# Performance work log

Hardware: AMD Instinct MI355X
Metric: run time of the kernel (lower is better)

Reference implementation:

```python
import jax, jax.numpy as jnp
import numpy as np
import math

N = 1024
C = 128
H = 4
HD = C // H  # 32
HID = C // 2  # geom_mlp hidden


def setup_inputs() -> dict:
    key = jax.random.key(0)
    ks = jax.random.split(key, 12)
    s = 0.02
    return {
        "x": jax.random.normal(ks[0], (N, C), jnp.float32),
        "y": jax.random.normal(ks[1], (N, C), jnp.float32),
        "pos": jax.random.normal(ks[2], (N, 3), jnp.float32),
        "Wq": jax.random.normal(ks[3], (C, C), jnp.float32) * s,
        "bq": jnp.zeros((C,), jnp.float32),
        "Wk": jax.random.normal(ks[4], (C, C), jnp.float32) * s,
        "bk": jnp.zeros((C,), jnp.float32),
        "Wv": jax.random.normal(ks[5], (C, C), jnp.float32) * s,
        "bv": jnp.zeros((C,), jnp.float32),
        "W1": jax.random.normal(ks[6], (3, HID), jnp.float32) * s,
        "b1": jnp.zeros((HID,), jnp.float32),
        "W2": jax.random.normal(ks[7], (HID, C), jnp.float32) * s,
        "b2": jnp.zeros((C,), jnp.float32),
    }


def _safe_norm(sq):
    # sqrt with zero (sub)gradient at 0, matching torch.norm behavior
    pos_mask = sq > 0
    return jnp.where(pos_mask, jnp.sqrt(jnp.where(pos_mask, sq, 1.0)), 0.0)


def reference(x, y, pos, Wq, bq, Wk, bk, Wv, bv, W1, b1, W2, b2):
    # pairwise geometry
    pos_diff = pos[:, None, :] - pos[None, :, :]          # [N, N, 3]
    dist = _safe_norm(jnp.sum(pos_diff * pos_diff, -1))   # [N, N]
    geom = jax.nn.relu(pos_diff @ W1 + b1) @ W2 + b2      # [N, N, C]
    geom = geom.reshape(N, N, H, HD)                      # per-head split

    q = (x @ Wq + bq).reshape(N, H, HD)
    k = (y @ Wk + bk).reshape(N, H, HD)
    v = (y @ Wv + bv).reshape(N, H, HD)

    attn = jnp.einsum("ihd,jhd->hij", q, k) / math.sqrt(HD)  # [H, N, N]
    geom_attn = jnp.einsum("ihd,ijhd->hij", q, geom)         # [H, N, N]
    scores = attn + geom_attn - dist[None, :, :]
    p = jax.nn.softmax(scores, axis=-1)
    out = jnp.einsum("hij,jhd->ihd", p, v).reshape(N, C)     # [N, C]
    return out
```

## Files before the change

### kernel.cpp

```cpp
#include <hip/hip_runtime.h>
#include <math.h>


typedef float v2f __attribute__((ext_vector_type(2)));
typedef float v4f __attribute__((ext_vector_type(4)));

#define L2E 1.4426950408889634f
#define RSL (0.17677669529663687f * L2E)

static __device__ __forceinline__ float dot4(float4 a, float4 b) {
  return a.x*b.x + a.y*b.y + a.z*b.z + a.w*b.w;
}
static __device__ __forceinline__ v2f fma2(v2f a, v2f b, v2f c) {
  return __builtin_elementwise_fma(a, b, c);
}
static __device__ __forceinline__ v4f fma4s(float s, v4f b, v4f c) {
  v4f sv = {s, s, s, s};
  return __builtin_elementwise_fma(sv, b, c);
}

__global__ __launch_bounds__(384) void k_pre(
    const float* __restrict__ x, const float* __restrict__ y, const float* __restrict__ pos,
    const float* __restrict__ Wq, const float* __restrict__ bq,
    const float* __restrict__ Wk, const float* __restrict__ bk,
    const float* __restrict__ Wv, const float* __restrict__ bv,
    const float* __restrict__ W1, const float* __restrict__ b1,
    const float* __restrict__ W2, const float* __restrict__ b2,
    float* __restrict__ q, float* __restrict__ v,
    float* __restrict__ kT4f, float* __restrict__ uT4f,
    float* __restrict__ sA, float* __restrict__ pos4w)
{
  __shared__ float xs[256], ys[256], qs[256];
  __shared__ __align__(16) float4 W2S[64*33];

  const int t  = threadIdx.x;
  const int n0 = blockIdx.x * 2;

  if (t < 256) { xs[t] = x[n0*128 + t]; ys[t] = y[n0*128 + t]; }
  {
    const float4* w2g = (const float4*)W2;
    #pragma unroll
    for (int r = 0; r < 6; ++r) {
      const int e = t + 384*r;
      if (e < 2048) W2S[(e>>5)*33 + (e&31)] = w2g[e];
    }
  }
  __syncthreads();

  {
    const int c   = t & 127;
    const int mat = t >> 7;
    const float* W    = (mat == 0) ? Wq : (mat == 1 ? Wk : Wv);
    const float* S    = (mat == 0) ? xs : ys;
    const float* bias = (mat == 0) ? bq : (mat == 1 ? bk : bv);
    float a0 = 0.f, a1 = 0.f;
    #pragma unroll 8
    for (int d = 0; d < 128; ++d) {
      const float w_ = W[d*128 + c];
      a0 = fmaf(S[d],       w_, a0);
      a1 = fmaf(S[128 + d], w_, a1);
    }
    const float bb = bias[c];
    a0 += bb; a1 += bb;
    if (mat == 0) {
      q[n0*128 + c] = a0 * RSL; q[(n0+1)*128 + c] = a1 * RSL;
      qs[c] = a0; qs[128 + c] = a1;
    } else if (mat == 2) {
      v[n0*128 + c] = a0; v[(n0+1)*128 + c] = a1;
    } else {
      kT4f[((c>>2)*1024 + n0  )*4 + (c&3)] = a0;
      kT4f[((c>>2)*1024 + n0+1)*4 + (c&3)] = a1;
    }
  }
  __syncthreads();

  if (t < 256) {
    const int m = t & 63, h = t >> 6;
    const float4* qs4 = (const float4*)qs;
    #pragma unroll
    for (int ii = 0; ii < 2; ++ii) {
      float acc = 0.f;
      #pragma unroll
      for (int ch = 0; ch < 8; ++ch)
        acc += dot4(qs4[ii*32 + h*8 + ch], W2S[m*33 + h*8 + ch]);
      sA[(n0+ii)*328 + 8 + (m>>2)*20 + h*4 + (m&3)] = acc * L2E;
    }
    if (t < 8) {
      const int ii = t >> 2, h2 = t & 3;
      float ca = 0.f;
      #pragma unroll
      for (int d = 0; d < 32; ++d) ca = fmaf(qs[ii*128 + h2*32 + d], b2[h2*32 + d], ca);
      sA[(n0+ii)*328 + h2] = ca * L2E;
    } else if (t < 16) {
      const int tt = t-8, ii = tt>>2, cc = tt&3;
      sA[(n0+ii)*328 + 4 + cc] = (cc < 3) ? pos[(n0+ii)*3 + cc] * L2E : 0.f;
    } else if (t < 24) {
      const int tt = t-16, ii = tt>>2, cc = tt&3;
      pos4w[(n0+ii)*4 + cc] = (cc < 3) ? pos[(n0+ii)*3 + cc] * L2E : 0.f;
    }
  } else {
    const int tt = t - 256, ii = tt >> 6, m = tt & 63;
    float ua = 0.f;
    #pragma unroll
    for (int cc = 0; cc < 3; ++cc) ua = fmaf(pos[(n0+ii)*3 + cc], W1[cc*64 + m], ua);
    uT4f[((m>>2)*1024 + (n0+ii))*4 + (m&3)] = ua;
    sA[(n0+ii)*328 + 8 + (m>>2)*20 + 16 + (m&3)] = ua + b1[m];
  }
}

__global__ __launch_bounds__(512, 4) void k_attn(
    const float* __restrict__ q, const float* __restrict__ v,
    const v4f* __restrict__ kT4, const v4f* __restrict__ uT4,
    const float* __restrict__ sA, const v4f* __restrict__ pos4,
    float* __restrict__ out)
{
  __shared__ __align__(16) float eL[8*544];
  __shared__ __align__(16) float rnum[4096];
  __shared__ float rden[64];

  const int t    = threadIdx.x;
  const int i0   = blockIdx.x * 2;
  const int w    = t >> 6;
  const int lane = t & 63;
  const int c4   = lane & 31;
  const int rep  = lane >> 5;
  const int hh   = c4 >> 3;

  const float* sA0 = sA + i0*328;
  const float* sA1 = sA0 + 328;
  const float* q0  = q + i0*128;
  const float* q1  = q0 + 128;

  const float c00 = sA0[0], c01 = sA0[1], c02 = sA0[2], c03 = sA0[3];
  const float c10 = sA1[0], c11 = sA1[1], c12 = sA1[2], c13 = sA1[3];
  const float p0x = sA0[4], p0y = sA0[5], p0z = sA0[6];
  const float p1x = sA1[4], p1y = sA1[5], p1z = sA1[6];

  v4f acc0 = {0.f,0.f,0.f,0.f};
  v4f acc1 = {0.f,0.f,0.f,0.f};
  float lsum[8] = {0.f,0.f,0.f,0.f,0.f,0.f,0.f,0.f};

  float* eW = &eL[w*544];
  const v4f* er0 = (const v4f*)&eL[w*544 +  hh     *68 + rep*32];
  const v4f* er1 = (const v4f*)&eL[w*544 + (4+hh)  *68 + rep*32];

  #pragma unroll
  for (int tt2 = 0; tt2 < 2; ++tt2) {
    const int jb = (w*2 + tt2) * 64;
    const int j  = jb + lane;

    const v4f pj = pos4[j];
    const float d0x = p0x-pj.x, d0y = p0y-pj.y, d0z = p0z-pj.z;
    const float d1x = p1x-pj.x, d1y = p1y-pj.y, d1z = p1z-pj.z;
    const float dist0 = sqrtf(d0x*d0x + d0y*d0y + d0z*d0z);
    const float dist1 = sqrtf(d1x*d1x + d1y*d1y + d1z*d1z);

    v2f g0a={0.f,0.f}, g0b={0.f,0.f}, g0c={0.f,0.f}, g0d={0.f,0.f};
    v2f g1a={0.f,0.f}, g1b={0.f,0.f}, g1c={0.f,0.f}, g1d={0.f,0.f};
    #pragma unroll 4
    for (int mb = 0; mb < 16; ++mb) {
      const v4f uj = uT4[mb*1024 + j];
      const v2f uj01 = uj.xy, uj23 = uj.zw;
      {
        const float* ab = sA0 + 8 + mb*20;
        const v2f z = {0.f, 0.f};
        const v2f h01 = __builtin_elementwise_max(*(const v2f*)(ab+16) - uj01, z);
        const v2f h23 = __builtin_elementwise_max(*(const v2f*)(ab+18) - uj23, z);
        g0a = fma2(h01, *(const v2f*)(ab+ 0), g0a); g0a = fma2(h23, *(const v2f*)(ab+ 2), g0a);
        g0b = fma2(h01, *(const v2f*)(ab+ 4), g0b); g0b = fma2(h23, *(const v2f*)(ab+ 6), g0b);
        g0c = fma2(h01, *(const v2f*)(ab+ 8), g0c); g0c = fma2(h23, *(const v2f*)(ab+10), g0c);
        g0d = fma2(h01, *(const v2f*)(ab+12), g0d); g0d = fma2(h23, *(const v2f*)(ab+14), g0d);
      }
      {
        const float* ab = sA1 + 8 + mb*20;
        const v2f z = {0.f, 0.f};
        const v2f h01 = __builtin_elementwise_max(*(const v2f*)(ab+16) - uj01, z);
        const v2f h23 = __builtin_elementwise_max(*(const v2f*)(ab+18) - uj23, z);
        g1a = fma2(h01, *(const v2f*)(ab+ 0), g1a); g1a = fma2(h23, *(const v2f*)(ab+ 2), g1a);
        g1b = fma2(h01, *(const v2f*)(ab+ 4), g1b); g1b = fma2(h23, *(const v2f*)(ab+ 6), g1b);
        g1c = fma2(h01, *(const v2f*)(ab+ 8), g1c); g1c = fma2(h23, *(const v2f*)(ab+10), g1c);
        g1d = fma2(h01, *(const v2f*)(ab+12), g1d); g1d = fma2(h23, *(const v2f*)(ab+14), g1d);
      }
    }

    v2f s0a={0.f,0.f}, s0b={0.f,0.f}, s0c={0.f,0.f}, s0d={0.f,0.f};
    v2f s1a={0.f,0.f}, s1b={0.f,0.f}, s1c={0.f,0.f}, s1d={0.f,0.f};
    #pragma unroll 8
    for (int cb = 0; cb < 8; ++cb) {
      const v4f k0 = kT4[(cb     )*1024 + j];
      const v4f k1 = kT4[(cb +  8)*1024 + j];
      const v4f k2 = kT4[(cb + 16)*1024 + j];
      const v4f k3 = kT4[(cb + 24)*1024 + j];
      s0a = fma2(k0.xy, *(const v2f*)(q0 + cb*4      ), s0a); s0a = fma2(k0.zw, *(const v2f*)(q0 + cb*4 +  2), s0a);
      s0b = fma2(k1.xy, *(const v2f*)(q0 + cb*4 + 32 ), s0b); s0b = fma2(k1.zw, *(const v2f*)(q0 + cb*4 + 34), s0b);
      s0c = fma2(k2.xy, *(const v2f*)(q0 + cb*4 + 64 ), s0c); s0c = fma2(k2.zw, *(const v2f*)(q0 + cb*4 + 66), s0c);
      s0d = fma2(k3.xy, *(const v2f*)(q0 + cb*4 + 96 ), s0d); s0d = fma2(k3.zw, *(const v2f*)(q0 + cb*4 + 98), s0d);
      s1a = fma2(k0.xy, *(const v2f*)(q1 + cb*4      ), s1a); s1a = fma2(k0.zw, *(const v2f*)(q1 + cb*4 +  2), s1a);
      s1b = fma2(k1.xy, *(const v2f*)(q1 + cb*4 + 32 ), s1b); s1b = fma2(k1.zw, *(const v2f*)(q1 + cb*4 + 34), s1b);
      s1c = fma2(k2.xy, *(const v2f*)(q1 + cb*4 + 64 ), s1c); s1c = fma2(k2.zw, *(const v2f*)(q1 + cb*4 + 66), s1c);
      s1d = fma2(k3.xy, *(const v2f*)(q1 + cb*4 + 96 ), s1d); s1d = fma2(k3.zw, *(const v2f*)(q1 + cb*4 + 98), s1d);
    }

    {
      const v2f t0a = s0a + g0a, t0b = s0b + g0b, t0c = s0c + g0c, t0d = s0d + g0d;
      const float p0 = exp2f(t0a.x + t0a.y + (c00 - dist0));
      const float p1 = exp2f(t0b.x + t0b.y + (c01 - dist0));
      const float p2 = exp2f(t0c.x + t0c.y + (c02 - dist0));
      const float p3 = exp2f(t0d.x + t0d.y + (c03 - dist0));
      lsum[0] += p0; lsum[1] += p1; lsum[2] += p2; lsum[3] += p3;
      eW[      lane] = p0; eW[ 68 + lane] = p1; eW[136 + lane] = p2; eW[204 + lane] = p3;
      const v2f t1a = s1a + g1a, t1b = s1b + g1b, t1c = s1c + g1c, t1d = s1d + g1d;
      const float r0 = exp2f(t1a.x + t1a.y + (c10 - dist1));
      const float r1 = exp2f(t1b.x + t1b.y + (c11 - dist1));
      const float r2 = exp2f(t1c.x + t1c.y + (c12 - dist1));
      const float r3 = exp2f(t1d.x + t1d.y + (c13 - dist1));
      lsum[4] += r0; lsum[5] += r1; lsum[6] += r2; lsum[7] += r3;
      eW[272 + lane] = r0; eW[340 + lane] = r1; eW[408 + lane] = r2; eW[476 + lane] = r3;
    }
    __builtin_amdgcn_wave_barrier();

    const v4f* vg = (const v4f*)(v + jb*128);
    const int vbase = rep*32*32 + c4;
    #pragma unroll 4
    for (int jj4 = 0; jj4 < 8; ++jj4) {
      const v4f e0 = er0[jj4];
      const v4f e1 = er1[jj4];
      const v4f va = vg[vbase + (jj4*4+0)*32];
      const v4f vb = vg[vbase + (jj4*4+1)*32];
      const v4f vc = vg[vbase + (jj4*4+2)*32];
      const v4f vd = vg[vbase + (jj4*4+3)*32];
      acc0 = fma4s(e0.x, va, acc0); acc1 = fma4s(e1.x, va, acc1);
      acc0 = fma4s(e0.y, vb, acc0); acc1 = fma4s(e1.y, vb, acc1);
      acc0 = fma4s(e0.z, vc, acc0); acc1 = fma4s(e1.z, vc, acc1);
      acc0 = fma4s(e0.w, vd, acc0); acc1 = fma4s(e1.w, vd, acc1);
    }
    __builtin_amdgcn_wave_barrier();
  }

  #pragma unroll
  for (int mm = 1; mm < 64; mm <<= 1) {
    #pragma unroll
    for (int r8 = 0; r8 < 8; ++r8) lsum[r8] += __shfl_xor(lsum[r8], mm);
  }
  ((v4f*)rnum)[((w*2+0)*2 + rep)*32 + c4] = acc0;
  ((v4f*)rnum)[((w*2+1)*2 + rep)*32 + c4] = acc1;
  if (lane == 0) {
    #pragma unroll
    for (int r8 = 0; r8 < 8; ++r8) rden[w*8 + r8] = lsum[r8];
  }
  __syncthreads();

  if (t < 256) {
    const int ii = t >> 7, c = t & 127;
    float num = 0.f, den = 0.f;
    #pragma unroll
    for (int ww = 0; ww < 8; ++ww) {
      num += rnum[((ww*2+ii)*2+0)*128 + c] + rnum[((ww*2+ii)*2+1)*128 + c];
      den += rden[ww*8 + ii*4 + (c>>5)];
    }
    out[(i0+ii)*128 + c] = num / den;
  }
}

extern "C" void kernel_launch(void* const* d_in, const int* in_sizes, int n_in,
                              void* d_out, int out_size, void* d_ws, size_t ws_size,
                              hipStream_t stream) {
  const float* x   = (const float*)d_in[0];
  const float* y   = (const float*)d_in[1];
  const float* pos = (const float*)d_in[2];
  const float* Wq  = (const float*)d_in[3];
  const float* bq  = (const float*)d_in[4];
  const float* Wk  = (const float*)d_in[5];
  const float* bk  = (const float*)d_in[6];
  const float* Wv  = (const float*)d_in[7];
  const float* bv  = (const float*)d_in[8];
  const float* W1  = (const float*)d_in[9];
  const float* b1  = (const float*)d_in[10];
  const float* W2  = (const float*)d_in[11];
  const float* b2  = (const float*)d_in[12];

  float* ws = (float*)d_ws;
  float* q    = ws;
  float* v    = ws + 131072;
  float* kT4f = ws + 262144;
  float* uT4f = ws + 393216;
  float* sA   = ws + 458752;
  float* pos4 = ws + 794624;
  float* out  = (float*)d_out;

  k_pre<<<dim3(512), dim3(384), 0, stream>>>(x, y, pos, Wq, bq, Wk, bk, Wv, bv,
                                             W1, b1, W2, b2,
                                             q, v, kT4f, uT4f, sA, pos4);
  k_attn<<<dim3(512), dim3(512), 0, stream>>>(q, v, (const v4f*)kT4f,
                                              (const v4f*)uT4f, sA,
                                              (const v4f*)pos4, out);
}
```

Before: 117.1 us.

## Process four query rows per block and split keys across two blocks

The attention kernel now handles four query rows per block, so each key, u and v load is reused across four rows instead of two. The key range is split between two blocks with one 64-key tile per wave. Partial numerators and denominators go to a workspace, and a new finalize kernel combines them. The precompute kernel is also changed to four rows per block. This roughly doubles per-thread accumulator registers, which risks lower occupancy or spills, and it adds a kernel launch plus a workspace round trip.

```diff
diff --git a/kernel.cpp b/kernel.cpp
--- a/kernel.cpp
+++ b/kernel.cpp
@@ -30,13 +30,13 @@
     float* __restrict__ kT4f, float* __restrict__ uT4f,
     float* __restrict__ sA, float* __restrict__ pos4w)
 {
-  __shared__ float xs[256], ys[256], qs[256];
+  __shared__ float xs[512], ys[512], qs[512];
   __shared__ __align__(16) float4 W2S[64*33];
 
   const int t  = threadIdx.x;
-  const int n0 = blockIdx.x * 2;
-
-  if (t < 256) { xs[t] = x[n0*128 + t]; ys[t] = y[n0*128 + t]; }
+  const int n0 = blockIdx.x * 4;
+
+  for (int idx = t; idx < 512; idx += 384) { xs[idx] = x[n0*128 + idx]; ys[idx] = y[n0*128 + idx]; }
   {
     const float4* w2g = (const float4*)W2;
     #pragma unroll
@@ -53,23 +53,29 @@
     const float* W    = (mat == 0) ? Wq : (mat == 1 ? Wk : Wv);
     const float* S    = (mat == 0) ? xs : ys;
     const float* bias = (mat == 0) ? bq : (mat == 1 ? bk : bv);
-    float a0 = 0.f, a1 = 0.f;
-    #pragma unroll 8
+    float a0=0.f, a1=0.f, a2=0.f, a3=0.f;
+    #pragma unroll 4
     for (int d = 0; d < 128; ++d) {
       const float w_ = W[d*128 + c];
-      a0 = fmaf(S[d],       w_, a0);
-      a1 = fmaf(S[128 + d], w_, a1);
+      a0 = fmaf(S[d],     w_, a0);
+      a1 = fmaf(S[128+d], w_, a1);
+      a2 = fmaf(S[256+d], w_, a2);
+      a3 = fmaf(S[384+d], w_, a3);
     }
     const float bb = bias[c];
-    a0 += bb; a1 += bb;
+    a0 += bb; a1 += bb; a2 += bb; a3 += bb;
     if (mat == 0) {
-      q[n0*128 + c] = a0 * RSL; q[(n0+1)*128 + c] = a1 * RSL;
-      qs[c] = a0; qs[128 + c] = a1;
+      q[(n0+0)*128+c] = a0*RSL; q[(n0+1)*128+c] = a1*RSL;
+      q[(n0+2)*128+c] = a2*RSL; q[(n0+3)*128+c] = a3*RSL;
+      qs[c] = a0; qs[128+c] = a1; qs[256+c] = a2; qs[384+c] = a3;
     } else if (mat == 2) {
-      v[n0*128 + c] = a0; v[(n0+1)*128 + c] = a1;
+      v[(n0+0)*128+c] = a0; v[(n0+1)*128+c] = a1;
+      v[(n0+2)*128+c] = a2; v[(n0+3)*128+c] = a3;
     } else {
-      kT4f[((c>>2)*1024 + n0  )*4 + (c&3)] = a0;
+      kT4f[((c>>2)*1024 + n0+0)*4 + (c&3)] = a0;
       kT4f[((c>>2)*1024 + n0+1)*4 + (c&3)] = a1;
+      kT4f[((c>>2)*1024 + n0+2)*4 + (c&3)] = a2;
+      kT4f[((c>>2)*1024 + n0+3)*4 + (c&3)] = a3;
     }
   }
   __syncthreads();
@@ -78,33 +84,38 @@
     const int m = t & 63, h = t >> 6;
     const float4* qs4 = (const float4*)qs;
     #pragma unroll
-    for (int ii = 0; ii < 2; ++ii) {
+    for (int ii = 0; ii < 4; ++ii) {
       float acc = 0.f;
       #pragma unroll
       for (int ch = 0; ch < 8; ++ch)
         acc += dot4(qs4[ii*32 + h*8 + ch], W2S[m*33 + h*8 + ch]);
       sA[(n0+ii)*328 + 8 + (m>>2)*20 + h*4 + (m&3)] = acc * L2E;
     }
-    if (t < 8) {
+    if (t < 16) {
       const int ii = t >> 2, h2 = t & 3;
       float ca = 0.f;
       #pragma unroll
       for (int d = 0; d < 32; ++d) ca = fmaf(qs[ii*128 + h2*32 + d], b2[h2*32 + d], ca);
       sA[(n0+ii)*328 + h2] = ca * L2E;
-    } else if (t < 16) {
-      const int tt = t-8, ii = tt>>2, cc = tt&3;
+    } else if (t < 32) {
+      const int tt = t-16, ii = tt>>2, cc = tt&3;
       sA[(n0+ii)*328 + 4 + cc] = (cc < 3) ? pos[(n0+ii)*3 + cc] * L2E : 0.f;
-    } else if (t < 24) {
-      const int tt = t-16, ii = tt>>2, cc = tt&3;
+    } else if (t < 48) {
+      const int tt = t-32, ii = tt>>2, cc = tt&3;
       pos4w[(n0+ii)*4 + cc] = (cc < 3) ? pos[(n0+ii)*3 + cc] * L2E : 0.f;
     }
   } else {
-    const int tt = t - 256, ii = tt >> 6, m = tt & 63;
-    float ua = 0.f;
-    #pragma unroll
-    for (int cc = 0; cc < 3; ++cc) ua = fmaf(pos[(n0+ii)*3 + cc], W1[cc*64 + m], ua);
-    uT4f[((m>>2)*1024 + (n0+ii))*4 + (m&3)] = ua;
-    sA[(n0+ii)*328 + 8 + (m>>2)*20 + 16 + (m&3)] = ua + b1[m];
+    const int tt = t - 256;
+    #pragma unroll
+    for (int rep = 0; rep < 2; ++rep) {
+      const int e = tt + 128*rep;
+      const int ii = e >> 6, m = e & 63;
+      float ua = 0.f;
+      #pragma unroll
+      for (int cc = 0; cc < 3; ++cc) ua = fmaf(pos[(n0+ii)*3 + cc], W1[cc*64 + m], ua);
+      uT4f[((m>>2)*1024 + (n0+ii))*4 + (m&3)] = ua;
+      sA[(n0+ii)*328 + 8 + (m>>2)*20 + 16 + (m&3)] = ua + b1[m];
+    }
   }
 }
 
@@ -112,154 +123,167 @@
     const float* __restrict__ q, const float* __restrict__ v,
     const v4f* __restrict__ kT4, const v4f* __restrict__ uT4,
     const float* __restrict__ sA, const v4f* __restrict__ pos4,
-    float* __restrict__ out)
+    float* __restrict__ wsP)
 {
-  __shared__ __align__(16) float eL[8*544];
-  __shared__ __align__(16) float rnum[4096];
-  __shared__ float rden[64];
-
-  const int t    = threadIdx.x;
-  const int i0   = blockIdx.x * 2;
-  const int w    = t >> 6;
-  const int lane = t & 63;
-  const int c4   = lane & 31;
-  const int rep  = lane >> 5;
-  const int hh   = c4 >> 3;
-
-  const float* sA0 = sA + i0*328;
-  const float* sA1 = sA0 + 328;
-  const float* q0  = q + i0*128;
-  const float* q1  = q0 + 128;
-
-  const float c00 = sA0[0], c01 = sA0[1], c02 = sA0[2], c03 = sA0[3];
-  const float c10 = sA1[0], c11 = sA1[1], c12 = sA1[2], c13 = sA1[3];
-  const float p0x = sA0[4], p0y = sA0[5], p0z = sA0[6];
-  const float p1x = sA1[4], p1y = sA1[5], p1z = sA1[6];
-
-  v4f acc0 = {0.f,0.f,0.f,0.f};
-  v4f acc1 = {0.f,0.f,0.f,0.f};
-  float lsum[8] = {0.f,0.f,0.f,0.f,0.f,0.f,0.f,0.f};
-
-  float* eW = &eL[w*544];
-  const v4f* er0 = (const v4f*)&eL[w*544 +  hh     *68 + rep*32];
-  const v4f* er1 = (const v4f*)&eL[w*544 + (4+hh)  *68 + rep*32];
-
-  #pragma unroll
-  for (int tt2 = 0; tt2 < 2; ++tt2) {
-    const int jb = (w*2 + tt2) * 64;
-    const int j  = jb + lane;
-
-    const v4f pj = pos4[j];
-    const float d0x = p0x-pj.x, d0y = p0y-pj.y, d0z = p0z-pj.z;
-    const float d1x = p1x-pj.x, d1y = p1y-pj.y, d1z = p1z-pj.z;
-    const float dist0 = sqrtf(d0x*d0x + d0y*d0y + d0z*d0z);
-    const float dist1 = sqrtf(d1x*d1x + d1y*d1y + d1z*d1z);
-
-    v2f g0a={0.f,0.f}, g0b={0.f,0.f}, g0c={0.f,0.f}, g0d={0.f,0.f};
-    v2f g1a={0.f,0.f}, g1b={0.f,0.f}, g1c={0.f,0.f}, g1d={0.f,0.f};
-    #pragma unroll 4
-    for (int mb = 0; mb < 16; ++mb) {
-      const v4f uj = uT4[mb*1024 + j];
-      const v2f uj01 = uj.xy, uj23 = uj.zw;
-      {
-        const float* ab = sA0 + 8 + mb*20;
-        const v2f z = {0.f, 0.f};
-        const v2f h01 = __builtin_elementwise_max(*(const v2f*)(ab+16) - uj01, z);
-        const v2f h23 = __builtin_elementwise_max(*(const v2f*)(ab+18) - uj23, z);
-        g0a = fma2(h01, *(const v2f*)(ab+ 0), g0a); g0a = fma2(h23, *(const v2f*)(ab+ 2), g0a);
-        g0b = fma2(h01, *(const v2f*)(ab+ 4), g0b); g0b = fma2(h23, *(const v2f*)(ab+ 6), g0b);
-        g0c = fma2(h01, *(const v2f*)(ab+ 8), g0c); g0c = fma2(h23, *(const v2f*)(ab+10), g0c);
-        g0d = fma2(h01, *(const v2f*)(ab+12), g0d); g0d = fma2(h23, *(const v2f*)(ab+14), g0d);
-      }
-      {
-        const float* ab = sA1 + 8 + mb*20;
-        const v2f z = {0.f, 0.f};
-        const v2f h01 = __builtin_elementwise_max(*(const v2f*)(ab+16) - uj01, z);
-        const v2f h23 = __builtin_elementwise_max(*(const v2f*)(ab+18) - uj23, z);
-        g1a = fma2(h01, *(const v2f*)(ab+ 0), g1a); g1a = fma2(h23, *(const v2f*)(ab+ 2), g1a);
-        g1b = fma2(h01, *(const v2f*)(ab+ 4), g1b); g1b = fma2(h23, *(const v2f*)(ab+ 6), g1b);
-        g1c = fma2(h01, *(const v2f*)(ab+ 8), g1c); g1c = fma2(h23, *(const v2f*)(ab+10), g1c);
-        g1d = fma2(h01, *(const v2f*)(ab+12), g1d); g1d = fma2(h23, *(const v2f*)(ab+14), g1d);
-      }
-    }
-
-    v2f s0a={0.f,0.f}, s0b={0.f,0.f}, s0c={0.f,0.f}, s0d={0.f,0.f};
-    v2f s1a={0.f,0.f}, s1b={0.f,0.f}, s1c={0.f,0.f}, s1d={0.f,0.f};
-    #pragma unroll 8
-    for (int cb = 0; cb < 8; ++cb) {
-      const v4f k0 = kT4[(cb     )*1024 + j];
-      const v4f k1 = kT4[(cb +  8)*1024 + j];
-      const v4f k2 = kT4[(cb + 16)*1024 + j];
-      const v4f k3 = kT4[(cb + 24)*1024 + j];
-      s0a = fma2(k0.xy, *(const v2f*)(q0 + cb*4      ), s0a); s0a = fma2(k0.zw, *(const v2f*)(q0 + cb*4 +  2), s0a);
-      s0b = fma2(k1.xy, *(const v2f*)(q0 + cb*4 + 32 ), s0b); s0b = fma2(k1.zw, *(const v2f*)(q0 + cb*4 + 34), s0b);
-      s0c = fma2(k2.xy, *(const v2f*)(q0 + cb*4 + 64 ), s0c); s0c = fma2(k2.zw, *(const v2f*)(q0 + cb*4 + 66), s0c);
-      s0d = fma2(k3.xy, *(const v2f*)(q0 + cb*4 + 96 ), s0d); s0d = fma2(k3.zw, *(const v2f*)(q0 + cb*4 + 98), s0d);
-      s1a = fma2(k0.xy, *(const v2f*)(q1 + cb*4      ), s1a); s1a = fma2(k0.zw, *(const v2f*)(q1 + cb*4 +  2), s1a);
-      s1b = fma2(k1.xy, *(const v2f*)(q1 + cb*4 + 32 ), s1b); s1b = fma2(k1.zw, *(const v2f*)(q1 + cb*4 + 34), s1b);
-      s1c = fma2(k2.xy, *(const v2f*)(q1 + cb*4 + 64 ), s1c); s1c = fma2(k2.zw, *(const v2f*)(q1 + cb*4 + 66), s1c);
-      s1d = fma2(k3.xy, *(const v2f*)(q1 + cb*4 + 96 ), s1d); s1d = fma2(k3.zw, *(const v2f*)(q1 + cb*4 + 98), s1d);
-    }
-
-    {
-      const v2f t0a = s0a + g0a, t0b = s0b + g0b, t0c = s0c + g0c, t0d = s0d + g0d;
-      const float p0 = exp2f(t0a.x + t0a.y + (c00 - dist0));
-      const float p1 = exp2f(t0b.x + t0b.y + (c01 - dist0));
-      const float p2 = exp2f(t0c.x + t0c.y + (c02 - dist0));
-      const float p3 = exp2f(t0d.x + t0d.y + (c03 - dist0));
-      lsum[0] += p0; lsum[1] += p1; lsum[2] += p2; lsum[3] += p3;
-      eW[      lane] = p0; eW[ 68 + lane] = p1; eW[136 + lane] = p2; eW[204 + lane] = p3;
-      const v2f t1a = s1a + g1a, t1b = s1b + g1b, t1c = s1c + g1c, t1d = s1d + g1d;
-      const float r0 = exp2f(t1a.x + t1a.y + (c10 - dist1));
-      const float r1 = exp2f(t1b.x + t1b.y + (c11 - dist1));
-      const float r2 = exp2f(t1c.x + t1c.y + (c12 - dist1));
-      const float r3 = exp2f(t1d.x + t1d.y + (c13 - dist1));
-      lsum[4] += r0; lsum[5] += r1; lsum[6] += r2; lsum[7] += r3;
-      eW[272 + lane] = r0; eW[340 + lane] = r1; eW[408 + lane] = r2; eW[476 + lane] = r3;
-    }
-    __builtin_amdgcn_wave_barrier();
-
+  __shared__ __align__(16) float eL[8*1088];
+  __shared__ __align__(16) float rnum[8192];
+  __shared__ float rden[128];
+
+  const int t     = threadIdx.x;
+  const int i0    = (blockIdx.x >> 1) * 4;
+  const int jhalf = blockIdx.x & 1;
+  const int w     = t >> 6;
+  const int lane  = t & 63;
+  const int c4    = lane & 31;
+  const int rep   = lane >> 5;
+  const int hh    = c4 >> 3;
+
+  const int jt = jhalf*8 + w;
+  const int jb = jt*64;
+  const int j  = jb + lane;
+
+  const float* sAi[4];
+  const float* qi[4];
+  #pragma unroll
+  for (int ii = 0; ii < 4; ++ii) { sAi[ii] = sA + (i0+ii)*328; qi[ii] = q + (i0+ii)*128; }
+
+  const v4f pj = pos4[j];
+  float dist[4];
+  #pragma unroll
+  for (int ii = 0; ii < 4; ++ii) {
+    const float dx = sAi[ii][4]-pj.x, dy = sAi[ii][5]-pj.y, dz = sAi[ii][6]-pj.z;
+    dist[ii] = sqrtf(dx*dx + dy*dy + dz*dz);
+  }
+
+  v2f g[4][4];
+  #pragma unroll
+  for (int ii = 0; ii < 4; ++ii)
+    #pragma unroll
+    for (int h = 0; h < 4; ++h) g[ii][h] = (v2f){0.f, 0.f};
+
+  #pragma unroll 4
+  for (int mb = 0; mb < 16; ++mb) {
+    const v4f uj = uT4[mb*1024 + j];
+    const v2f uj01 = uj.xy, uj23 = uj.zw;
+    const v2f z = {0.f, 0.f};
+    #pragma unroll
+    for (int ii = 0; ii < 4; ++ii) {
+      const float* ab = sAi[ii] + 8 + mb*20;
+      const v2f h01 = __builtin_elementwise_max(*(const v2f*)(ab+16) - uj01, z);
+      const v2f h23 = __builtin_elementwise_max(*(const v2f*)(ab+18) - uj23, z);
+      g[ii][0] = fma2(h01, *(const v2f*)(ab+ 0), g[ii][0]); g[ii][0] = fma2(h23, *(const v2f*)(ab+ 2), g[ii][0]);
+      g[ii][1] = fma2(h01, *(const v2f*)(ab+ 4), g[ii][1]); g[ii][1] = fma2(h23, *(const v2f*)(ab+ 6), g[ii][1]);
+      g[ii][2] = fma2(h01, *(const v2f*)(ab+ 8), g[ii][2]); g[ii][2] = fma2(h23, *(const v2f*)(ab+10), g[ii][2]);
+      g[ii][3] = fma2(h01, *(const v2f*)(ab+12), g[ii][3]); g[ii][3] = fma2(h23, *(const v2f*)(ab+14), g[ii][3]);
+    }
+  }
+
+  v2f s[4][4];
+  #pragma unroll
+  for (int ii = 0; ii < 4; ++ii)
+    #pragma unroll
+    for (int h = 0; h < 4; ++h) s[ii][h] = (v2f){0.f, 0.f};
+
+  #pragma unroll 4
+  for (int cb = 0; cb < 8; ++cb) {
+    const v4f k0 = kT4[(cb     )*1024 + j];
+    const v4f k1 = kT4[(cb +  8)*1024 + j];
+    const v4f k2 = kT4[(cb + 16)*1024 + j];
+    const v4f k3 = kT4[(cb + 24)*1024 + j];
+    #pragma unroll
+    for (int ii = 0; ii < 4; ++ii) {
+      const float* qq = qi[ii] + cb*4;
+      s[ii][0] = fma2(k0.xy, *(const v2f*)(qq     ), s[ii][0]); s[ii][0] = fma2(k0.zw, *(const v2f*)(qq +  2), s[ii][0]);
+      s[ii][1] = fma2(k1.xy, *(const v2f*)(qq + 32), s[ii][1]); s[ii][1] = fma2(k1.zw, *(const v2f*)(qq + 34), s[ii][1]);
+      s[ii][2] = fma2(k2.xy, *(const v2f*)(qq + 64), s[ii][2]); s[ii][2] = fma2(k2.zw, *(const v2f*)(qq + 66), s[ii][2]);
+      s[ii][3] = fma2(k3.xy, *(const v2f*)(qq + 96), s[ii][3]); s[ii][3] = fma2(k3.zw, *(const v2f*)(qq + 98), s[ii][3]);
+    }
+  }
+
+  float lsum[16];
+  float* eW = &eL[w*1088];
+  #pragma unroll
+  for (int ii = 0; ii < 4; ++ii) {
+    #pragma unroll
+    for (int h = 0; h < 4; ++h) {
+      const v2f tt = s[ii][h] + g[ii][h];
+      const float p = exp2f(tt.x + tt.y + (sAi[ii][h] - dist[ii]));
+      lsum[ii*4+h] = p;
+      eW[(ii*4+h)*68 + lane] = p;
+    }
+  }
+  __builtin_amdgcn_wave_barrier();
+
+  v4f acc[4] = {{0.f,0.f,0.f,0.f},{0.f,0.f,0.f,0.f},{0.f,0.f,0.f,0.f},{0.f,0.f,0.f,0.f}};
+  {
     const v4f* vg = (const v4f*)(v + jb*128);
     const int vbase = rep*32*32 + c4;
+    const v4f* er[4];
+    #pragma unroll
+    for (int ii = 0; ii < 4; ++ii)
+      er[ii] = (const v4f*)&eL[w*1088 + (ii*4+hh)*68 + rep*32];
     #pragma unroll 4
     for (int jj4 = 0; jj4 < 8; ++jj4) {
-      const v4f e0 = er0[jj4];
-      const v4f e1 = er1[jj4];
       const v4f va = vg[vbase + (jj4*4+0)*32];
       const v4f vb = vg[vbase + (jj4*4+1)*32];
       const v4f vc = vg[vbase + (jj4*4+2)*32];
       const v4f vd = vg[vbase + (jj4*4+3)*32];
-      acc0 = fma4s(e0.x, va, acc0); acc1 = fma4s(e1.x, va, acc1);
-      acc0 = fma4s(e0.y, vb, acc0); acc1 = fma4s(e1.y, vb, acc1);
-      acc0 = fma4s(e0.z, vc, acc0); acc1 = fma4s(e1.z, vc, acc1);
-      acc0 = fma4s(e0.w, vd, acc0); acc1 = fma4s(e1.w, vd, acc1);
-    }
-    __builtin_amdgcn_wave_barrier();
-  }
-
-  #pragma unroll
-  for (int mm = 1; mm < 64; mm <<= 1) {
-    #pragma unroll
-    for (int r8 = 0; r8 < 8; ++r8) lsum[r8] += __shfl_xor(lsum[r8], mm);
-  }
-  ((v4f*)rnum)[((w*2+0)*2 + rep)*32 + c4] = acc0;
-  ((v4f*)rnum)[((w*2+1)*2 + rep)*32 + c4] = acc1;
+      #pragma unroll
+      for (int ii = 0; ii < 4; ++ii) {
+        const v4f e4 = er[ii][jj4];
+        acc[ii] = fma4s(e4.x, va, acc[ii]);
+        acc[ii] = fma4s(e4.y, vb, acc[ii]);
+        acc[ii] = fma4s(e4.z, vc, acc[ii]);
+        acc[ii] = fma4s(e4.w, vd, acc[ii]);
+      }
+    }
+  }
+  __builtin_amdgcn_wave_barrier();
+
+  #pragma unroll
+  for (int mm = 1; mm < 64; mm <<= 1)
+    #pragma unroll
+    for (int r16 = 0; r16 < 16; ++r16) lsum[r16] += __shfl_xor(lsum[r16], mm);
+
+  #pragma unroll
+  for (int ii = 0; ii < 4; ++ii)
+    ((v4f*)rnum)[((w*4 + ii)*2 + rep)*32 + c4] = acc[ii];
   if (lane == 0) {
     #pragma unroll
-    for (int r8 = 0; r8 < 8; ++r8) rden[w*8 + r8] = lsum[r8];
+    for (int r16 = 0; r16 < 16; ++r16) rden[w*16 + r16] = lsum[r16];
   }
   __syncthreads();
 
-  if (t < 256) {
+  float* P = wsP + (size_t)blockIdx.x * 528;
+  {
     const int ii = t >> 7, c = t & 127;
-    float num = 0.f, den = 0.f;
+    float num = 0.f;
     #pragma unroll
     for (int ww = 0; ww < 8; ++ww) {
-      num += rnum[((ww*2+ii)*2+0)*128 + c] + rnum[((ww*2+ii)*2+1)*128 + c];
-      den += rden[ww*8 + ii*4 + (c>>5)];
-    }
-    out[(i0+ii)*128 + c] = num / den;
-  }
+      num += rnum[((ww*4+ii)*2+0)*128 + c];
+      num += rnum[((ww*4+ii)*2+1)*128 + c];
+    }
+    P[ii*128 + c] = num;
+  }
+  if (t < 16) {
+    float den = 0.f;
+    #pragma unroll
+    for (int ww = 0; ww < 8; ++ww) den += rden[ww*16 + t];
+    P[512 + t] = den;
+  }
+}
+
+__global__ __launch_bounds__(512) void k_fin(const float* __restrict__ wsP,
+                                             float* __restrict__ out)
+{
+  const int gid = blockIdx.x * 512 + threadIdx.x;
+  const int i = gid >> 7, c = gid & 127;
+  const int gq = i >> 2, ii = i & 3;
+  const float* P0 = wsP + (size_t)(gq*2+0) * 528;
+  const float* P1 = wsP + (size_t)(gq*2+1) * 528;
+  const float num = P0[ii*128 + c] + P1[ii*128 + c];
+  const float den = P0[512 + ii*4 + (c>>5)] + P1[512 + ii*4 + (c>>5)];
+  out[gid] = num / den;
 }
 
 extern "C" void kernel_launch(void* const* d_in, const int* in_sizes, int n_in,
@@ -286,12 +310,14 @@
   float* uT4f = ws + 393216;
   float* sA   = ws + 458752;
   float* pos4 = ws + 794624;
+  float* wsP  = ws + 798720;
   float* out  = (float*)d_out;
 
-  k_pre<<<dim3(512), dim3(384), 0, stream>>>(x, y, pos, Wq, bq, Wk, bk, Wv, bv,
+  k_pre<<<dim3(256), dim3(384), 0, stream>>>(x, y, pos, Wq, bq, Wk, bk, Wv, bv,
                                              W1, b1, W2, b2,
                                              q, v, kT4f, uT4f, sA, pos4);
   k_attn<<<dim3(512), dim3(512), 0, stream>>>(q, v, (const v4f*)kT4f,
                                               (const v4f*)uT4f, sA,
-                                              (const v4f*)pos4, out);
-}
+                                              (const v4f*)pos4, wsP);
+  k_fin<<<dim3(256), dim3(512), 0, stream>>>(wsP, out);
+}
```

Measured after the change: 141.8 us. +21.0%, slower.

## Split attention key range across two blocks and combine partials in finalize kernel

Applied to the files above, without the earlier changes.

Each query pair is now handled by two blocks, each covering half of the 1024 keys, so every wave processes one 64-key tile instead of looping over two. Partial numerators and denominators go to workspace, and a new finalize kernel sums them and divides. This doubles the grid to 1024 blocks and raises the launch-bounds occupancy hint to improve latency hiding. The cost is an extra kernel launch and a round trip of partial results through global memory.

```diff
diff --git a/kernel.cpp b/kernel.cpp
--- a/kernel.cpp
+++ b/kernel.cpp
@@ -108,23 +108,28 @@
   }
 }
 
-__global__ __launch_bounds__(512, 4) void k_attn(
+__global__ __launch_bounds__(512, 8) void k_attn(
     const float* __restrict__ q, const float* __restrict__ v,
     const v4f* __restrict__ kT4, const v4f* __restrict__ uT4,
     const float* __restrict__ sA, const v4f* __restrict__ pos4,
-    float* __restrict__ out)
+    float* __restrict__ wsP)
 {
   __shared__ __align__(16) float eL[8*544];
   __shared__ __align__(16) float rnum[4096];
   __shared__ float rden[64];
 
-  const int t    = threadIdx.x;
-  const int i0   = blockIdx.x * 2;
-  const int w    = t >> 6;
-  const int lane = t & 63;
-  const int c4   = lane & 31;
-  const int rep  = lane >> 5;
-  const int hh   = c4 >> 3;
+  const int t     = threadIdx.x;
+  const int i0    = (blockIdx.x >> 1) * 2;
+  const int jhalf = blockIdx.x & 1;
+  const int w     = t >> 6;
+  const int lane  = t & 63;
+  const int c4    = lane & 31;
+  const int rep   = lane >> 5;
+  const int hh    = c4 >> 3;
+
+  const int jt = jhalf*8 + w;
+  const int jb = jt*64;
+  const int j  = jb + lane;
 
   const float* sA0 = sA + i0*328;
   const float* sA1 = sA0 + 328;
@@ -136,89 +141,82 @@
   const float p0x = sA0[4], p0y = sA0[5], p0z = sA0[6];
   const float p1x = sA1[4], p1y = sA1[5], p1z = sA1[6];
 
+  const v4f pj = pos4[j];
+  const float d0x = p0x-pj.x, d0y = p0y-pj.y, d0z = p0z-pj.z;
+  const float d1x = p1x-pj.x, d1y = p1y-pj.y, d1z = p1z-pj.z;
+  const float dist0 = sqrtf(d0x*d0x + d0y*d0y + d0z*d0z);
+  const float dist1 = sqrtf(d1x*d1x + d1y*d1y + d1z*d1z);
+
+  v2f g0a={0.f,0.f}, g0b={0.f,0.f}, g0c={0.f,0.f}, g0d={0.f,0.f};
+  v2f g1a={0.f,0.f}, g1b={0.f,0.f}, g1c={0.f,0.f}, g1d={0.f,0.f};
+  #pragma unroll 4
+  for (int mb = 0; mb < 16; ++mb) {
+    const v4f uj = uT4[mb*1024 + j];
+    const v2f uj01 = uj.xy, uj23 = uj.zw;
+    const v2f z = {0.f, 0.f};
+    {
+      const float* ab = sA0 + 8 + mb*20;
+      const v2f h01 = __builtin_elementwise_max(*(const v2f*)(ab+16) - uj01, z);
+      const v2f h23 = __builtin_elementwise_max(*(const v2f*)(ab+18) - uj23, z);
+      g0a = fma2(h01, *(const v2f*)(ab+ 0), g0a); g0a = fma2(h23, *(const v2f*)(ab+ 2), g0a);
+      g0b = fma2(h01, *(const v2f*)(ab+ 4), g0b); g0b = fma2(h23, *(const v2f*)(ab+ 6), g0b);
+      g0c = fma2(h01, *(const v2f*)(ab+ 8), g0c); g0c = fma2(h23, *(const v2f*)(ab+10), g0c);
+      g0d = fma2(h01, *(const v2f*)(ab+12), g0d); g0d = fma2(h23, *(const v2f*)(ab+14), g0d);
+    }
+    {
+      const float* ab = sA1 + 8 + mb*20;
+      const v2f h01 = __builtin_elementwise_max(*(const v2f*)(ab+16) - uj01, z);
+      const v2f h23 = __builtin_elementwise_max(*(const v2f*)(ab+18) - uj23, z);
+      g1a = fma2(h01, *(const v2f*)(ab+ 0), g1a); g1a = fma2(h23, *(const v2f*)(ab+ 2), g1a);
+      g1b = fma2(h01, *(const v2f*)(ab+ 4), g1b); g1b = fma2(h23, *(const v2f*)(ab+ 6), g1b);
+      g1c = fma2(h01, *(const v2f*)(ab+ 8), g1c); g1c = fma2(h23, *(const v2f*)(ab+10), g1c);
+      g1d = fma2(h01, *(const v2f*)(ab+12), g1d); g1d = fma2(h23, *(const v2f*)(ab+14), g1d);
+    }
+  }
+
+  v2f s0a={0.f,0.f}, s0b={0.f,0.f}, s0c={0.f,0.f}, s0d={0.f,0.f};
+  v2f s1a={0.f,0.f}, s1b={0.f,0.f}, s1c={0.f,0.f}, s1d={0.f,0.f};
+  #pragma unroll 8
+  for (int cb = 0; cb < 8; ++cb) {
+    const v4f k0 = kT4[(cb     )*1024 + j];
+    const v4f k1 = kT4[(cb +  8)*1024 + j];
+    const v4f k2 = kT4[(cb + 16)*1024 + j];
+    const v4f k3 = kT4[(cb + 24)*1024 + j];
+    s0a = fma2(k0.xy, *(const v2f*)(q0 + cb*4      ), s0a); s0a = fma2(k0.zw, *(const v2f*)(q0 + cb*4 +  2), s0a);
+    s0b = fma2(k1.xy, *(const v2f*)(q0 + cb*4 + 32 ), s0b); s0b = fma2(k1.zw, *(const v2f*)(q0 + cb*4 + 34), s0b);
+    s0c = fma2(k2.xy, *(const v2f*)(q0 + cb*4 + 64 ), s0c); s0c = fma2(k2.zw, *(const v2f*)(q0 + cb*4 + 66), s0c);
+    s0d = fma2(k3.xy, *(const v2f*)(q0 + cb*4 + 96 ), s0d); s0d = fma2(k3.zw, *(const v2f*)(q0 + cb*4 + 98), s0d);
+    s1a = fma2(k0.xy, *(const v2f*)(q1 + cb*4      ), s1a); s1a = fma2(k0.zw, *(const v2f*)(q1 + cb*4 +  2), s1a);
+    s1b = fma2(k1.xy, *(const v2f*)(q1 + cb*4 + 32 ), s1b); s1b = fma2(k1.zw, *(const v2f*)(q1 + cb*4 + 34), s1b);
+    s1c = fma2(k2.xy, *(const v2f*)(q1 + cb*4 + 64 ), s1c); s1c = fma2(k2.zw, *(const v2f*)(q1 + cb*4 + 66), s1c);
+    s1d = fma2(k3.xy, *(const v2f*)(q1 + cb*4 + 96 ), s1d); s1d = fma2(k3.zw, *(const v2f*)(q1 + cb*4 + 98), s1d);
+  }
+
+  float lsum[8];
+  float* eW = &eL[w*544];
+  {
+    const v2f t0a = s0a + g0a, t0b = s0b + g0b, t0c = s0c + g0c, t0d = s0d + g0d;
+    const float p0 = exp2f(t0a.x + t0a.y + (c00 - dist0));
+    const float p1 = exp2f(t0b.x + t0b.y + (c01 - dist0));
+    const float p2 = exp2f(t0c.x + t0c.y + (c02 - dist0));
+    const float p3 = exp2f(t0d.x + t0d.y + (c03 - dist0));
+    lsum[0] = p0; lsum[1] = p1; lsum[2] = p2; lsum[3] = p3;
+    eW[      lane] = p0; eW[ 68 + lane] = p1; eW[136 + lane] = p2; eW[204 + lane] = p3;
+    const v2f t1a = s1a + g1a, t1b = s1b + g1b, t1c = s1c + g1c, t1d = s1d + g1d;
+    const float r0 = exp2f(t1a.x + t1a.y + (c10 - dist1));
+    const float r1 = exp2f(t1b.x + t1b.y + (c11 - dist1));
+    const float r2 = exp2f(t1c.x + t1c.y + (c12 - dist1));
+    const float r3 = exp2f(t1d.x + t1d.y + (c13 - dist1));
+    lsum[4] = r0; lsum[5] = r1; lsum[6] = r2; lsum[7] = r3;
+    eW[272 + lane] = r0; eW[340 + lane] = r1; eW[408 + lane] = r2; eW[476 + lane] = r3;
+  }
+  __builtin_amdgcn_wave_barrier();
+
   v4f acc0 = {0.f,0.f,0.f,0.f};
   v4f acc1 = {0.f,0.f,0.f,0.f};
-  float lsum[8] = {0.f,0.f,0.f,0.f,0.f,0.f,0.f,0.f};
-
-  float* eW = &eL[w*544];
-  const v4f* er0 = (const v4f*)&eL[w*544 +  hh     *68 + rep*32];
-  const v4f* er1 = (const v4f*)&eL[w*544 + (4+hh)  *68 + rep*32];
-
-  #pragma unroll
-  for (int tt2 = 0; tt2 < 2; ++tt2) {
-    const int jb = (w*2 + tt2) * 64;
-    const int j  = jb + lane;
-
-    const v4f pj = pos4[j];
-    const float d0x = p0x-pj.x, d0y = p0y-pj.y, d0z = p0z-pj.z;
-    const float d1x = p1x-pj.x, d1y = p1y-pj.y, d1z = p1z-pj.z;
-    const float dist0 = sqrtf(d0x*d0x + d0y*d0y + d0z*d0z);
-    const float dist1 = sqrtf(d1x*d1x + d1y*d1y + d1z*d1z);
-
-    v2f g0a={0.f,0.f}, g0b={0.f,0.f}, g0c={0.f,0.f}, g0d={0.f,0.f};
-    v2f g1a={0.f,0.f}, g1b={0.f,0.f}, g1c={0.f,0.f}, g1d={0.f,0.f};
-    #pragma unroll 4
-    for (int mb = 0; mb < 16; ++mb) {
-      const v4f uj = uT4[mb*1024 + j];
-      const v2f uj01 = uj.xy, uj23 = uj.zw;
-      {
-        const float* ab = sA0 + 8 + mb*20;
-        const v2f z = {0.f, 0.f};
-        const v2f h01 = __builtin_elementwise_max(*(const v2f*)(ab+16) - uj01, z);
-        const v2f h23 = __builtin_elementwise_max(*(const v2f*)(ab+18) - uj23, z);
-        g0a = fma2(h01, *(const v2f*)(ab+ 0), g0a); g0a = fma2(h23, *(const v2f*)(ab+ 2), g0a);
-        g0b = fma2(h01, *(const v2f*)(ab+ 4), g0b); g0b = fma2(h23, *(const v2f*)(ab+ 6), g0b);
-        g0c = fma2(h01, *(const v2f*)(ab+ 8), g0c); g0c = fma2(h23, *(const v2f*)(ab+10), g0c);
-        g0d = fma2(h01, *(const v2f*)(ab+12), g0d); g0d = fma2(h23, *(const v2f*)(ab+14), g0d);
-      }
-      {
-        const float* ab = sA1 + 8 + mb*20;
-        const v2f z = {0.f, 0.f};
-        const v2f h01 = __builtin_elementwise_max(*(const v2f*)(ab+16) - uj01, z);
-        const v2f h23 = __builtin_elementwise_max(*(const v2f*)(ab+18) - uj23, z);
-        g1a = fma2(h01, *(const v2f*)(ab+ 0), g1a); g1a = fma2(h23, *(const v2f*)(ab+ 2), g1a);
-        g1b = fma2(h01, *(const v2f*)(ab+ 4), g1b); g1b = fma2(h23, *(const v2f*)(ab+ 6), g1b);
-        g1c = fma2(h01, *(const v2f*)(ab+ 8), g1c); g1c = fma2(h23, *(const v2f*)(ab+10), g1c);
-        g1d = fma2(h01, *(const v2f*)(ab+12), g1d); g1d = fma2(h23, *(const v2f*)(ab+14), g1d);
-      }
-    }
-
-    v2f s0a={0.f,0.f}, s0b={0.f,0.f}, s0c={0.f,0.f}, s0d={0.f,0.f};
-    v2f s1a={0.f,0.f}, s1b={0.f,0.f}, s1c={0.f,0.f}, s1d={0.f,0.f};
-    #pragma unroll 8
-    for (int cb = 0; cb < 8; ++cb) {
-      const v4f k0 = kT4[(cb     )*1024 + j];
-      const v4f k1 = kT4[(cb +  8)*1024 + j];
-      const v4f k2 = kT4[(cb + 16)*1024 + j];
-      const v4f k3 = kT4[(cb + 24)*1024 + j];
-      s0a = fma2(k0.xy, *(const v2f*)(q0 + cb*4      ), s0a); s0a = fma2(k0.zw, *(const v2f*)(q0 + cb*4 +  2), s0a);
-      s0b = fma2(k1.xy, *(const v2f*)(q0 + cb*4 + 32 ), s0b); s0b = fma2(k1.zw, *(const v2f*)(q0 + cb*4 + 34), s0b);
-      s0c = fma2(k2.xy, *(const v2f*)(q0 + cb*4 + 64 ), s0c); s0c = fma2(k2.zw, *(const v2f*)(q0 + cb*4 + 66), s0c);
-      s0d = fma2(k3.xy, *(const v2f*)(q0 + cb*4 + 96 ), s0d); s0d = fma2(k3.zw, *(const v2f*)(q0 + cb*4 + 98), s0d);
-      s1a = fma2(k0.xy, *(const v2f*)(q1 + cb*4      ), s1a); s1a = fma2(k0.zw, *(const v2f*)(q1 + cb*4 +  2), s1a);
-      s1b = fma2(k1.xy, *(const v2f*)(q1 + cb*4 + 32 ), s1b); s1b = fma2(k1.zw, *(const v2f*)(q1 + cb*4 + 34), s1b);
-      s1c = fma2(k2.xy, *(const v2f*)(q1 + cb*4 + 64 ), s1c); s1c = fma2(k2.zw, *(const v2f*)(q1 + cb*4 + 66), s1c);
-      s1d = fma2(k3.xy, *(const v2f*)(q1 + cb*4 + 96 ), s1d); s1d = fma2(k3.zw, *(const v2f*)(q1 + cb*4 + 98), s1d);
-    }
-
-    {
-      const v2f t0a = s0a + g0a, t0b = s0b + g0b, t0c = s0c + g0c, t0d = s0d + g0d;
-      const float p0 = exp2f(t0a.x + t0a.y + (c00 - dist0));
-      const float p1 = exp2f(t0b.x + t0b.y + (c01 - dist0));
-      const float p2 = exp2f(t0c.x + t0c.y + (c02 - dist0));
-      const float p3 = exp2f(t0d.x + t0d.y + (c03 - dist0));
-      lsum[0] += p0; lsum[1] += p1; lsum[2] += p2; lsum[3] += p3;
-      eW[      lane] = p0; eW[ 68 + lane] = p1; eW[136 + lane] = p2; eW[204 + lane] = p3;
-      const v2f t1a = s1a + g1a, t1b = s1b + g1b, t1c = s1c + g1c, t1d = s1d + g1d;
-      const float r0 = exp2f(t1a.x + t1a.y + (c10 - dist1));
-      const float r1 = exp2f(t1b.x + t1b.y + (c11 - dist1));
-      const float r2 = exp2f(t1c.x + t1c.y + (c12 - dist1));
-      const float r3 = exp2f(t1d.x + t1d.y + (c13 - dist1));
-      lsum[4] += r0; lsum[5] += r1; lsum[6] += r2; lsum[7] += r3;
-      eW[272 + lane] = r0; eW[340 + lane] = r1; eW[408 + lane] = r2; eW[476 + lane] = r3;
-    }
-    __builtin_amdgcn_wave_barrier();
-
+  {
+    const v4f* er0 = (const v4f*)&eL[w*544 +  hh    *68 + rep*32];
+    const v4f* er1 = (const v4f*)&eL[w*544 + (4+hh) *68 + rep*32];
     const v4f* vg = (const v4f*)(v + jb*128);
     const int vbase = rep*32*32 + c4;
     #pragma unroll 4
@@ -234,8 +232,8 @@
       acc0 = fma4s(e0.z, vc, acc0); acc1 = fma4s(e1.z, vc, acc1);
       acc0 = fma4s(e0.w, vd, acc0); acc1 = fma4s(e1.w, vd, acc1);
     }
-    __builtin_amdgcn_wave_barrier();
-  }
+  }
+  __builtin_amdgcn_wave_barrier();
 
   #pragma unroll
   for (int mm = 1; mm < 64; mm <<= 1) {
@@ -250,16 +248,37 @@
   }
   __syncthreads();
 
+  float* P = wsP + (size_t)blockIdx.x * 264;
   if (t < 256) {
     const int ii = t >> 7, c = t & 127;
-    float num = 0.f, den = 0.f;
+    float num = 0.f;
     #pragma unroll
     for (int ww = 0; ww < 8; ++ww) {
-      num += rnum[((ww*2+ii)*2+0)*128 + c] + rnum[((ww*2+ii)*2+1)*128 + c];
-      den += rden[ww*8 + ii*4 + (c>>5)];
-    }
-    out[(i0+ii)*128 + c] = num / den;
-  }
+      num += rnum[((ww*2+ii)*2+0)*128 + c];
+      num += rnum[((ww*2+ii)*2+1)*128 + c];
+    }
+    P[ii*128 + c] = num;
+  }
+  if (t >= 256 && t < 264) {
+    const int r8 = t - 256;
+    float den = 0.f;
+    #pragma unroll
+    for (int ww = 0; ww < 8; ++ww) den += rden[ww*8 + r8];
+    P[256 + r8] = den;
+  }
+}
+
+__global__ __launch_bounds__(512) void k_fin(const float* __restrict__ wsP,
+                                             float* __restrict__ out)
+{
+  const int gid = blockIdx.x * 512 + threadIdx.x;
+  const int i = gid >> 7, c = gid & 127;
+  const int ipair = i >> 1, ii = i & 1;
+  const float* P0 = wsP + (size_t)(ipair*2+0) * 264;
+  const float* P1 = wsP + (size_t)(ipair*2+1) * 264;
+  const float num = P0[ii*128 + c] + P1[ii*128 + c];
+  const float den = P0[256 + ii*4 + (c>>5)] + P1[256 + ii*4 + (c>>5)];
+  out[gid] = num / den;
 }
 
 extern "C" void kernel_launch(void* const* d_in, const int* in_sizes, int n_in,
@@ -286,12 +305,14 @@
   float* uT4f = ws + 393216;
   float* sA   = ws + 458752;
   float* pos4 = ws + 794624;
+  float* wsP  = ws + 798720;
   float* out  = (float*)d_out;
 
   k_pre<<<dim3(512), dim3(384), 0, stream>>>(x, y, pos, Wq, bq, Wk, bk, Wv, bv,
                                              W1, b1, W2, b2,
                                              q, v, kT4f, uT4f, sA, pos4);
-  k_attn<<<dim3(512), dim3(512), 0, stream>>>(q, v, (const v4f*)kT4f,
-                                              (const v4f*)uT4f, sA,
-                                              (const v4f*)pos4, out);
-}
+  k_attn<<<dim3(1024), dim3(512), 0, stream>>>(q, v, (const v4f*)kT4f,
+                                               (const v4f*)uT4f, sA,
+                                               (const v4f*)pos4, wsP);
+  k_fin<<<dim3(256), dim3(512), 0, stream>>>(wsP, out);
+}
```

Result: slower. 120.0 us (+2.5%).
